# Kernel optimization log

Hardware: AMD Instinct MI355X
Metric: run time of the kernel (lower is better)

Reference implementation:

```python
import jax, jax.numpy as jnp
import numpy as np
import math

B, M, H, K, SPAN = 8, 1024, 512, 8, 1024
D = H // K
MK = M + SPAN


def _skew(X, pad_value):
    # shift every row one step to the right: [N, M, L] -> [N, M, M+L]
    N, m, L = X.shape
    X = jnp.pad(X, ((0, 0), (0, 0), (0, m + 1)), constant_values=pad_value)
    X = X.reshape(N, -1)[:, :-m]
    return X.reshape(N, m, m + L)


def _unskew(X):
    # reverse of _skew: [N, M, M+L] -> [N, M, L]
    N, m, Lk = X.shape
    L = Lk - m
    X = jnp.pad(X.reshape(N, -1), ((0, 0), (0, m)))
    return X.reshape(N, m, Lk + 1)[:, :, :L]


def setup_inputs() -> dict:
    key0 = jax.random.key(0)
    ks = jax.random.split(key0, 8)
    w_scale = 1.0 / math.sqrt(H)
    return {
        "query": jax.random.normal(ks[0], (B, M, H), jnp.float32),
        "key": jax.random.normal(ks[1], (B, MK, H), jnp.float32),
        "value": jax.random.normal(ks[2], (B, MK, H), jnp.float32),
        "pos_encoding": jax.random.normal(ks[3], (D, SPAN), jnp.float32) * w_scale,
        "Wq": jax.random.normal(ks[4], (H, H), jnp.float32) * w_scale,
        "Wk": jax.random.normal(ks[5], (H, H), jnp.float32) * w_scale,
        "Wv": jax.random.normal(ks[6], (H, H), jnp.float32) * w_scale,
        "Wo": jax.random.normal(ks[7], (H, H), jnp.float32) * w_scale,
    }


def _heads(x, W):
    # project then split heads: [B, T, H] -> [B*K, T, D]
    x = x @ W
    Bx, T, _ = x.shape
    x = x.reshape(Bx, T, K, D).transpose(0, 2, 1, 3)
    return x.reshape(Bx * K, T, D)


def reference(query, key, value, pos_encoding, Wq, Wk, Wv, Wo):
    q = _heads(query, Wq)      # [B*K, M, D]
    k = _heads(key, Wk)        # [B*K, MK, D]
    v = _heads(value, Wv)      # [B*K, MK, D]

    attn_ctx = jnp.einsum("nmd,nld->nml", q, k)   # [B*K, M, MK]
    attn_ctx = _unskew(attn_ctx)                    # [B*K, M, SPAN]
    attn_pos = jnp.einsum("nmd,ds->nms", q, pos_encoding)  # [B*K, M, SPAN]
    attn = jax.nn.softmax((attn_ctx + attn_pos) / math.sqrt(D), axis=-1)

    attn_sk = _skew(attn, 0.0)                      # [B*K, M, MK]
    out = jnp.einsum("nml,nld->nmd", attn_sk, v)   # [B*K, M, D]
    out = out.reshape(B, K, M, D).transpose(0, 2, 1, 3).reshape(B, M, H)
    return out @ Wo
```

## Files before the change

kernel.cpp:

```cpp
#include <hip/hip_runtime.h>
#include <stdint.h>

#define Bq 8
#define Mq 1024
#define Hq 512
#define NHq 8
#define Dq 64
#define SPANq 1024
#define MKq 2048
#define PR2 168

typedef __bf16 bf16x8 __attribute__((ext_vector_type(8)));
typedef _Float16 f16x8 __attribute__((ext_vector_type(8)));
typedef float f32x4 __attribute__((ext_vector_type(4)));
typedef unsigned short ushort8 __attribute__((ext_vector_type(8)));
typedef unsigned int uint2v __attribute__((ext_vector_type(2)));

static __device__ __forceinline__ unsigned short f2bf(float f) {
  union { float f; unsigned u; } x; x.f = f;
  unsigned r = x.u + 0x7FFFu + ((x.u >> 16) & 1u);
  return (unsigned short)(r >> 16);
}

static __device__ __forceinline__ unsigned pk_f16(float a, float b) {
  return __builtin_bit_cast(unsigned, __builtin_amdgcn_cvt_pkrtz(a, b));
}

static __device__ __forceinline__ f32x4 mfma_bf16(bf16x8 a, bf16x8 b, f32x4 c) {
  return __builtin_amdgcn_mfma_f32_16x16x32_bf16(a, b, c, 0, 0, 0);
}
static __device__ __forceinline__ f32x4 mfma_f16(f16x8 a, f16x8 b, f32x4 c) {
  return __builtin_amdgcn_mfma_f32_16x16x32_f16(a, b, c, 0, 0, 0);
}

static __device__ __forceinline__ void async_ld16(const void* g, void* l) {
  __builtin_amdgcn_global_load_lds(
      (const __attribute__((address_space(1))) void*)g,
      (__attribute__((address_space(3))) void*)l, 16, 0, 0);
}

__global__ __launch_bounds__(256) void prep_all(
    const float* __restrict__ query, const float* __restrict__ key,
    const float* __restrict__ value,
    const float* __restrict__ Wq, const float* __restrict__ Wk,
    const float* __restrict__ Wv, const float* __restrict__ Wo,
    const float* __restrict__ pos,
    unsigned short* __restrict__ qX, unsigned short* __restrict__ kX,
    unsigned short* __restrict__ vX,
    unsigned short* __restrict__ WTq, unsigned short* __restrict__ WTk,
    unsigned short* __restrict__ WTv, unsigned short* __restrict__ WTo,
    unsigned short* __restrict__ posT) {
  __shared__ float tile[64][65];
  const int bid = blockIdx.x;
  const int tid = threadIdx.x;
  if (bid >= 272) {
    const int rem = bid - 272;
    const float* src; unsigned short* dst; int off;
    if (rem < 2048)      { src = query; dst = qX; off = rem; }
    else if (rem < 6144) { src = key;   dst = kX; off = rem - 2048; }
    else                 { src = value; dst = vX; off = rem - 6144; }
    const int idx = off * 2048 + tid * 8;
    const f32x4 f0 = *(const f32x4*)(src + idx);
    const f32x4 f1 = *(const f32x4*)(src + idx + 4);
    ushort8 h;
    h[0] = f2bf(f0[0]); h[1] = f2bf(f0[1]); h[2] = f2bf(f0[2]); h[3] = f2bf(f0[3]);
    h[4] = f2bf(f1[0]); h[5] = f2bf(f1[1]); h[6] = f2bf(f1[2]); h[7] = f2bf(f1[3]);
    *(ushort8*)(dst + idx) = h;
    return;
  }
  const float* src; unsigned short* dst;
  int src_stride, dst_stride, i0, o0;
  if (bid < 256) {
    const int w = bid >> 6, t = bid & 63;
    src = (w == 0) ? Wq : (w == 1) ? Wk : (w == 2) ? Wv : Wo;
    dst = (w == 0) ? WTq : (w == 1) ? WTk : (w == 2) ? WTv : WTo;
    src_stride = Hq; dst_stride = Hq;
    i0 = (t >> 3) * 64; o0 = (t & 7) * 64;
  } else {
    const int t = bid - 256;
    src = pos; dst = posT;
    src_stride = SPANq; dst_stride = Dq;
    i0 = 0; o0 = t * 64;
  }
  for (int e = tid; e < 4096; e += 256) {
    const int r = e >> 6, c = e & 63;
    tile[r][c] = src[(size_t)(i0 + r) * src_stride + o0 + c];
  }
  __syncthreads();
  for (int e = tid; e < 4096; e += 256) {
    const int r = e >> 6, c = e & 63;
    dst[(size_t)(o0 + r) * dst_stride + i0 + c] = f2bf(tile[c][r]);
  }
}

static __device__ __forceinline__ void gemm_body(
    const unsigned short* __restrict__ Xb, const unsigned short* __restrict__ WT,
    unsigned short* __restrict__ outb, _Float16* __restrict__ outv,
    float* __restrict__ outf, int mode, int tshift, int bx, int by,
    unsigned short* sh) {
  unsigned short* As = sh;
  unsigned short* Bs = sh + 8192;
  const int tid = threadIdx.x;
  const int wave = tid >> 6, lane = tid & 63;
  const int q = lane >> 4, l16 = lane & 15;
  const int wy = wave >> 1, wx = wave & 1;
  const size_t m0 = (size_t)bx * 128;
  const int n0 = by * 128;
  const int dsub = lane >> 3;
  const int dswz = (lane & 7) ^ dsub;

  f32x4 acc[4][4] = {};

  for (int k0 = 0; k0 < Hq; k0 += 64) {
    __syncthreads();
#pragma unroll
    for (int i = 0; i < 4; i++) {
      const int s = wave * 4 + i;
      const int r = s * 8 + dsub;
      async_ld16(Xb + (m0 + r) * Hq + k0 + dswz * 8, As + s * 512);
      async_ld16(WT + (size_t)(n0 + r) * Hq + k0 + dswz * 8, Bs + s * 512);
    }
    __syncthreads();
#pragma unroll
    for (int h = 0; h < 2; h++) {
      bf16x8 af[4], bg[4];
#pragma unroll
      for (int mt = 0; mt < 4; mt++) {
        const int R = wy * 64 + mt * 16 + l16;
        af[mt] = *(const bf16x8*)(As + R * 64 + (((h * 4 + q) ^ (l16 & 7)) * 8));
      }
#pragma unroll
      for (int nt = 0; nt < 4; nt++) {
        const int R = wx * 64 + nt * 16 + l16;
        bg[nt] = *(const bf16x8*)(Bs + R * 64 + (((h * 4 + q) ^ (l16 & 7)) * 8));
      }
#pragma unroll
      for (int mt = 0; mt < 4; mt++)
#pragma unroll
        for (int nt = 0; nt < 4; nt++)
          acc[mt][nt] = mfma_bf16(af[mt], bg[nt], acc[mt][nt]);
    }
  }

  if (mode == 2) {
    __syncthreads();
    _Float16* tr = (_Float16*)sh + wave * 4608;
#pragma unroll
    for (int nt = 0; nt < 4; nt++)
#pragma unroll
      for (int mt = 0; mt < 4; mt++)
#pragma unroll
        for (int r = 0; r < 4; r++)
          tr[(nt * 16 + l16) * 72 + mt * 16 + q * 4 + r] = (_Float16)acc[mt][nt][r];
    const int head = by * 2 + wx;
    const int mrow0 = (int)m0 + wy * 64;
    const int Tlen = 1 << tshift;
    const int b = mrow0 >> tshift, t0 = mrow0 & (Tlen - 1);
#pragma unroll
    for (int it = 0; it < 8; it++) {
      const int dl = it * 8 + (lane >> 3), tl = (lane & 7) * 8;
      const f16x8 v = *(const f16x8*)(tr + dl * 72 + tl);
      *(f16x8*)(outv + ((size_t)((b * 8 + head) * 64 + dl)) * Tlen + t0 + tl) = v;
    }
    return;
  }

  const int Tlen = 1 << tshift;
#pragma unroll
  for (int mt = 0; mt < 4; mt++) {
#pragma unroll
    for (int nt = 0; nt < 4; nt++) {
      const int c = n0 + wx * 64 + nt * 16 + l16;
#pragma unroll
      for (int r = 0; r < 4; r++) {
        const int m = (int)m0 + wy * 64 + mt * 16 + q * 4 + r;
        const float val = acc[mt][nt][r];
        if (mode == 3) {
          outf[(size_t)m * Hq + c] = val;
        } else {
          const int b = m >> tshift, t = m & (Tlen - 1);
          const int head = c >> 6, d = c & 63;
          outb[(((size_t)(b * 8 + head) << tshift) + t) * 64 + d] = f2bf(val);
        }
      }
    }
  }
}

__global__ __launch_bounds__(256, 4) void gemm_qkv(
    const unsigned short* __restrict__ qX, const unsigned short* __restrict__ kX,
    const unsigned short* __restrict__ vX,
    const unsigned short* __restrict__ WTq, const unsigned short* __restrict__ WTk,
    const unsigned short* __restrict__ WTv,
    unsigned short* __restrict__ qb, unsigned short* __restrict__ kbuf,
    _Float16* __restrict__ vTb) {
  __shared__ unsigned short sh[18432];
  const int bid = blockIdx.x;
  if (bid < 256) {
    gemm_body(qX, WTq, qb, nullptr, nullptr, 0, 10, bid & 63, bid >> 6, sh);
  } else if (bid < 768) {
    const int b2 = bid - 256;
    gemm_body(kX, WTk, kbuf, nullptr, nullptr, 0, 11, b2 & 127, b2 >> 7, sh);
  } else {
    const int b2 = bid - 768;
    gemm_body(vX, WTv, nullptr, vTb, nullptr, 2, 11, b2 & 127, b2 >> 7, sh);
  }
}

__global__ __launch_bounds__(256, 4) void gemm_out(
    const unsigned short* __restrict__ ctx, const unsigned short* __restrict__ WTo,
    float* __restrict__ out) {
  __shared__ unsigned short sh[18432];
  const int bid = blockIdx.x;
  gemm_body(ctx, WTo, nullptr, nullptr, out, 3, 10, bid & 63, bid >> 6, sh);
}

__global__ __launch_bounds__(256, 2) void attn4(
    const unsigned short* __restrict__ qb, const unsigned short* __restrict__ kglob,
    const _Float16* __restrict__ vT, const unsigned short* __restrict__ posT,
    unsigned short* __restrict__ ctx) {
  __shared__ unsigned short Kt[12288];
  __shared__ unsigned short PosR[4 * 16 * PR2];
  __shared__ unsigned short Prow[4 * 16 * PR2];

  const int tid = threadIdx.x;
  const int wave = tid >> 6, lane = tid & 63;
  const int q = lane >> 4, l16 = lane & 15;
  const int bid = blockIdx.x;
  const int n = (bid & 7) * 8 + (bid >> 7);
  const int mtile = (bid >> 3) & 15;
  const int m0 = mtile * 64;
  const int m0w = m0 + wave * 16;
  const int dsub = lane >> 3;
  const int dswz = (lane & 7) ^ dsub;

  unsigned short* prow = Prow + (wave * 16 + l16) * PR2;
  unsigned short* posr = PosR + (wave * 16 + l16) * PR2;

  const unsigned short* qbase = qb + ((size_t)n * Mq + m0w + l16) * Dq;
  const bf16x8 qf0 = *(const bf16x8*)(qbase + q * 8);
  const bf16x8 qf1 = *(const bf16x8*)(qbase + 32 + q * 8);

  const unsigned short* kbn = kglob + (size_t)n * MKq * Dq;
  const _Float16* vbn = vT + (size_t)n * Dq * MKq;

  f32x4 O[4] = {};
  float zrow = 0.f, mrow = -1e30f;

#pragma unroll
  for (int i = 0; i < 6; i++) {
    const int s = wave + 4 * i;
    const int r = s * 8 + dsub;
    async_ld16(kbn + (size_t)(m0 + r) * Dq + dswz * 8, Kt + s * 512);
  }
  {
    bf16x8 pf[8][2];
#pragma unroll
    for (int t = 0; t < 8; t++) {
      const unsigned short* pp = posT + (size_t)(t * 16 + l16) * Dq + q * 8;
      pf[t][0] = *(const bf16x8*)pp;
      pf[t][1] = *(const bf16x8*)(pp + 32);
    }
#pragma unroll
    for (int t = 0; t < 8; t++) {
      f32x4 b = {};
      b = mfma_bf16(pf[t][0], qf0, b);
      b = mfma_bf16(pf[t][1], qf1, b);
      const int cw = 16 + t * 16 + 4 * q + l16;
      posr[cw + 0] = f2bf(b[0]);
      posr[cw + 1] = f2bf(b[1]);
      posr[cw + 2] = f2bf(b[2]);
      posr[cw + 3] = f2bf(b[3]);
    }
  }
  __syncthreads();

  for (int c = 0; c < 8; c++) {
    const int j00 = m0w + c * 128;

    f32x4 S[9];
#pragma unroll
    for (int t = 0; t < 9; t++) {
      const int rl = wave * 16 + t * 16 + l16;
      const int ch = (q ^ (l16 & 7)) * 8;
      const bf16x8 k0 = *(const bf16x8*)(Kt + rl * 64 + ch);
      const bf16x8 k1 = *(const bf16x8*)(Kt + rl * 64 + (ch ^ 32));
      f32x4 a = {};
      a = mfma_bf16(k0, qf0, a);
      a = mfma_bf16(k1, qf1, a);
      const uint2v pv = *(const uint2v*)(posr + 16 + t * 16 + 4 * q);
      a[0] += __uint_as_float(pv.x << 16);
      a[1] += __uint_as_float(pv.x & 0xffff0000u);
      a[2] += __uint_as_float(pv.y << 16);
      a[3] += __uint_as_float(pv.y & 0xffff0000u);
      S[t] = a;
    }
#pragma unroll
    for (int r = 0; r < 4; r++) {
      if (4 * q + r < l16) S[0][r] = -1e30f;
      if (4 * q + r >= l16) S[8][r] = -1e30f;
    }

    if (c < 7) {
      __syncthreads();
      const int jb1 = m0 + (c + 1) * 128;
#pragma unroll
      for (int i = 0; i < 6; i++) {
        const int s = wave + 4 * i;
        const int r = s * 8 + dsub;
        async_ld16(kbn + (size_t)(jb1 + r) * Dq + dswz * 8, Kt + s * 512);
      }
      const int sb1 = (c + 1) * 128;
      bf16x8 pf[8][2];
#pragma unroll
      for (int t = 0; t < 8; t++) {
        const unsigned short* pp = posT + (size_t)(sb1 + t * 16 + l16) * Dq + q * 8;
        pf[t][0] = *(const bf16x8*)pp;
        pf[t][1] = *(const bf16x8*)(pp + 32);
      }
#pragma unroll
      for (int t = 0; t < 8; t++) {
        f32x4 b = {};
        b = mfma_bf16(pf[t][0], qf0, b);
        b = mfma_bf16(pf[t][1], qf1, b);
        const int cw = 16 + t * 16 + 4 * q + l16;
        posr[cw + 0] = f2bf(b[0]);
        posr[cw + 1] = f2bf(b[1]);
        posr[cw + 2] = f2bf(b[2]);
        posr[cw + 3] = f2bf(b[3]);
      }
    }

    float mx = -1e30f;
#pragma unroll
    for (int t = 0; t < 9; t++)
      mx = fmaxf(mx, fmaxf(fmaxf(S[t][0], S[t][1]), fmaxf(S[t][2], S[t][3])));
    mx = fmaxf(mx, __shfl_xor(mx, 16, 64));
    mx = fmaxf(mx, __shfl_xor(mx, 32, 64));
    const float m_new = fmaxf(mrow, mx);
    const float alpha = __expf((mrow - m_new) * 0.125f);
    float zs = 0.f;
#pragma unroll
    for (int t = 0; t < 9; t++) {
#pragma unroll
      for (int r = 0; r < 4; r++) {
        const float e = __expf((S[t][r] - m_new) * 0.125f);
        S[t][r] = e; zs += e;
      }
    }
    zs += __shfl_xor(zs, 16, 64);
    zs += __shfl_xor(zs, 32, 64);
    zrow = zrow * alpha + zs;
    mrow = m_new;
#pragma unroll
    for (int dt = 0; dt < 4; dt++) O[dt] *= alpha;

#pragma unroll
    for (int t = 0; t < 9; t++) {
      *(unsigned*)(prow + t * 16 + 4 * q) = pk_f16(S[t][0], S[t][1]);
      *(unsigned*)(prow + t * 16 + 4 * q + 2) = pk_f16(S[t][2], S[t][3]);
    }
    *(unsigned*)(prow + 144 + 4 * q) = 0u;
    *(unsigned*)(prow + 144 + 4 * q + 2) = 0u;

    f16x8 Bf[5];
#pragma unroll
    for (int kt = 0; kt < 5; kt++)
      Bf[kt] = *(const f16x8*)(prow + kt * 32 + q * 8);
    f16x8 Vv[5][4];
#pragma unroll
    for (int kt = 0; kt < 5; kt++) {
      int j = j00 + kt * 32 + q * 8;
      if (j > MKq - 8) j = MKq - 8;
#pragma unroll
      for (int dt = 0; dt < 4; dt++)
        Vv[kt][dt] = *(const f16x8*)(vbn + (size_t)(dt * 16 + l16) * MKq + j);
    }
#pragma unroll
    for (int kt = 0; kt < 5; kt++)
#pragma unroll
      for (int dt = 0; dt < 4; dt++)
        O[dt] = mfma_f16(Vv[kt][dt], Bf[kt], O[dt]);

    if (c < 7) __syncthreads();
  }

  const float zi = 1.f / zrow;
  unsigned short* cp = ctx + ((size_t)(n >> 3) * Mq + m0w + l16) * Hq + (n & 7) * Dq;
#pragma unroll
  for (int dt = 0; dt < 4; dt++)
#pragma unroll
    for (int r = 0; r < 4; r++)
      cp[dt * 16 + q * 4 + r] = f2bf(O[dt][r] * zi);
}

extern "C" void kernel_launch(void* const* d_in, const int* in_sizes, int n_in,
                              void* d_out, int out_size, void* d_ws, size_t ws_size,
                              hipStream_t stream) {
  const float* query = (const float*)d_in[0];
  const float* key   = (const float*)d_in[1];
  const float* value = (const float*)d_in[2];
  const float* pos   = (const float*)d_in[3];
  const float* Wq    = (const float*)d_in[4];
  const float* Wk    = (const float*)d_in[5];
  const float* Wv    = (const float*)d_in[6];
  const float* Wo    = (const float*)d_in[7];
  float* out = (float*)d_out;

  char* w = (char*)d_ws;
  unsigned short* qX   = (unsigned short*)w; w += (size_t)Bq * Mq * Hq * 2;
  unsigned short* kX   = (unsigned short*)w; w += (size_t)Bq * MKq * Hq * 2;
  unsigned short* vX   = (unsigned short*)w; w += (size_t)Bq * MKq * Hq * 2;
  unsigned short* qb   = (unsigned short*)w; w += (size_t)64 * Mq * Dq * 2;
  unsigned short* kbuf = (unsigned short*)w; w += (size_t)64 * MKq * Dq * 2;
  _Float16*       vTb  = (_Float16*)w;       w += (size_t)64 * Dq * MKq * 2;
  unsigned short* posT = (unsigned short*)w; w += (size_t)SPANq * Dq * 2;
  unsigned short* WTq  = (unsigned short*)w; w += (size_t)Hq * Hq * 2;
  unsigned short* WTk  = (unsigned short*)w; w += (size_t)Hq * Hq * 2;
  unsigned short* WTv  = (unsigned short*)w; w += (size_t)Hq * Hq * 2;
  unsigned short* WTo  = (unsigned short*)w; w += (size_t)Hq * Hq * 2;
  unsigned short* ctx  = (unsigned short*)w; w += (size_t)Bq * Mq * Hq * 2;

  prep_all<<<10512, 256, 0, stream>>>(query, key, value, Wq, Wk, Wv, Wo, pos,
                                      qX, kX, vX, WTq, WTk, WTv, WTo, posT);
  gemm_qkv<<<1280, 256, 0, stream>>>(qX, kX, vX, WTq, WTk, WTv, qb, kbuf, vTb);
  attn4<<<1024, 256, 0, stream>>>(qb, kbuf, vTb, posT, ctx);
  gemm_out<<<256, 256, 0, stream>>>(ctx, WTo, out);
}
```

Measured before the change: 321.2 us.

## Drop shared K staging in attention, load K directly, raise occupancy

The attention kernel no longer stages K tiles into shared memory with async loads and block barriers. Each wave now reads its K rows straight from global memory into registers, and one shared row buffer serves both the position scores (now stored as fp16) and the probabilities. Loads are split into smaller groups to lower register pressure, and the launch bound rises to four blocks per CU. The GEMM inner loop is also reordered to keep fewer B fragments live. The aim is to remove barriers and LDS use in exchange for redundant global K reads across waves and lower precision for the position term.

Result: slower. 359.9 us (+12.1%).

```diff
diff --git a/kernel.cpp b/kernel.cpp
--- a/kernel.cpp
+++ b/kernel.cpp
@@ -24,6 +24,15 @@
 
 static __device__ __forceinline__ unsigned pk_f16(float a, float b) {
   return __builtin_bit_cast(unsigned, __builtin_amdgcn_cvt_pkrtz(a, b));
+}
+static __device__ __forceinline__ unsigned short f16b(float x) {
+  return __builtin_bit_cast(unsigned short, (_Float16)x);
+}
+static __device__ __forceinline__ float f16_lo(unsigned u) {
+  return (float)__builtin_bit_cast(_Float16, (unsigned short)(u & 0xffffu));
+}
+static __device__ __forceinline__ float f16_hi(unsigned u) {
+  return (float)__builtin_bit_cast(_Float16, (unsigned short)(u >> 16));
 }
 
 static __device__ __forceinline__ f32x4 mfma_bf16(bf16x8 a, bf16x8 b, f32x4 c) {
@@ -123,7 +132,7 @@
     __syncthreads();
 #pragma unroll
     for (int h = 0; h < 2; h++) {
-      bf16x8 af[4], bg[4];
+      bf16x8 af[4];
 #pragma unroll
       for (int mt = 0; mt < 4; mt++) {
         const int R = wy * 64 + mt * 16 + l16;
@@ -132,13 +141,11 @@
 #pragma unroll
       for (int nt = 0; nt < 4; nt++) {
         const int R = wx * 64 + nt * 16 + l16;
-        bg[nt] = *(const bf16x8*)(Bs + R * 64 + (((h * 4 + q) ^ (l16 & 7)) * 8));
-      }
-#pragma unroll
-      for (int mt = 0; mt < 4; mt++)
-#pragma unroll
-        for (int nt = 0; nt < 4; nt++)
-          acc[mt][nt] = mfma_bf16(af[mt], bg[nt], acc[mt][nt]);
+        const bf16x8 bg = *(const bf16x8*)(Bs + R * 64 + (((h * 4 + q) ^ (l16 & 7)) * 8));
+#pragma unroll
+        for (int mt = 0; mt < 4; mt++)
+          acc[mt][nt] = mfma_bf16(af[mt], bg, acc[mt][nt]);
+      }
     }
   }
 
@@ -215,13 +222,11 @@
   gemm_body(ctx, WTo, nullptr, nullptr, out, 3, 10, bid & 63, bid >> 6, sh);
 }
 
-__global__ __launch_bounds__(256, 2) void attn4(
+__global__ __launch_bounds__(256, 4) void attn5(
     const unsigned short* __restrict__ qb, const unsigned short* __restrict__ kglob,
     const _Float16* __restrict__ vT, const unsigned short* __restrict__ posT,
     unsigned short* __restrict__ ctx) {
-  __shared__ unsigned short Kt[12288];
-  __shared__ unsigned short PosR[4 * 16 * PR2];
-  __shared__ unsigned short Prow[4 * 16 * PR2];
+  __shared__ unsigned short Rows[4 * 16 * PR2];
 
   const int tid = threadIdx.x;
   const int wave = tid >> 6, lane = tid & 63;
@@ -229,13 +234,9 @@
   const int bid = blockIdx.x;
   const int n = (bid & 7) * 8 + (bid >> 7);
   const int mtile = (bid >> 3) & 15;
-  const int m0 = mtile * 64;
-  const int m0w = m0 + wave * 16;
-  const int dsub = lane >> 3;
-  const int dswz = (lane & 7) ^ dsub;
-
-  unsigned short* prow = Prow + (wave * 16 + l16) * PR2;
-  unsigned short* posr = PosR + (wave * 16 + l16) * PR2;
+  const int m0w = mtile * 64 + wave * 16;
+
+  unsigned short* row = Rows + (wave * 16 + l16) * PR2;
 
   const unsigned short* qbase = qb + ((size_t)n * Mq + m0w + l16) * Dq;
   const bf16x8 qf0 = *(const bf16x8*)(qbase + q * 8);
@@ -247,74 +248,15 @@
   f32x4 O[4] = {};
   float zrow = 0.f, mrow = -1e30f;
 
-#pragma unroll
-  for (int i = 0; i < 6; i++) {
-    const int s = wave + 4 * i;
-    const int r = s * 8 + dsub;
-    async_ld16(kbn + (size_t)(m0 + r) * Dq + dswz * 8, Kt + s * 512);
-  }
-  {
-    bf16x8 pf[8][2];
-#pragma unroll
-    for (int t = 0; t < 8; t++) {
-      const unsigned short* pp = posT + (size_t)(t * 16 + l16) * Dq + q * 8;
-      pf[t][0] = *(const bf16x8*)pp;
-      pf[t][1] = *(const bf16x8*)(pp + 32);
-    }
-#pragma unroll
-    for (int t = 0; t < 8; t++) {
-      f32x4 b = {};
-      b = mfma_bf16(pf[t][0], qf0, b);
-      b = mfma_bf16(pf[t][1], qf1, b);
-      const int cw = 16 + t * 16 + 4 * q + l16;
-      posr[cw + 0] = f2bf(b[0]);
-      posr[cw + 1] = f2bf(b[1]);
-      posr[cw + 2] = f2bf(b[2]);
-      posr[cw + 3] = f2bf(b[3]);
-    }
-  }
-  __syncthreads();
-
   for (int c = 0; c < 8; c++) {
-    const int j00 = m0w + c * 128;
-
-    f32x4 S[9];
-#pragma unroll
-    for (int t = 0; t < 9; t++) {
-      const int rl = wave * 16 + t * 16 + l16;
-      const int ch = (q ^ (l16 & 7)) * 8;
-      const bf16x8 k0 = *(const bf16x8*)(Kt + rl * 64 + ch);
-      const bf16x8 k1 = *(const bf16x8*)(Kt + rl * 64 + (ch ^ 32));
-      f32x4 a = {};
-      a = mfma_bf16(k0, qf0, a);
-      a = mfma_bf16(k1, qf1, a);
-      const uint2v pv = *(const uint2v*)(posr + 16 + t * 16 + 4 * q);
-      a[0] += __uint_as_float(pv.x << 16);
-      a[1] += __uint_as_float(pv.x & 0xffff0000u);
-      a[2] += __uint_as_float(pv.y << 16);
-      a[3] += __uint_as_float(pv.y & 0xffff0000u);
-      S[t] = a;
-    }
-#pragma unroll
-    for (int r = 0; r < 4; r++) {
-      if (4 * q + r < l16) S[0][r] = -1e30f;
-      if (4 * q + r >= l16) S[8][r] = -1e30f;
-    }
-
-    if (c < 7) {
-      __syncthreads();
-      const int jb1 = m0 + (c + 1) * 128;
-#pragma unroll
-      for (int i = 0; i < 6; i++) {
-        const int s = wave + 4 * i;
-        const int r = s * 8 + dsub;
-        async_ld16(kbn + (size_t)(jb1 + r) * Dq + dswz * 8, Kt + s * 512);
-      }
-      const int sb1 = (c + 1) * 128;
+    const int sbase = c * 128;
+    const int j00 = m0w + sbase;
+
+    {
       bf16x8 pf[8][2];
 #pragma unroll
       for (int t = 0; t < 8; t++) {
-        const unsigned short* pp = posT + (size_t)(sb1 + t * 16 + l16) * Dq + q * 8;
+        const unsigned short* pp = posT + (size_t)(sbase + t * 16 + l16) * Dq + q * 8;
         pf[t][0] = *(const bf16x8*)pp;
         pf[t][1] = *(const bf16x8*)(pp + 32);
       }
@@ -324,11 +266,59 @@
         b = mfma_bf16(pf[t][0], qf0, b);
         b = mfma_bf16(pf[t][1], qf1, b);
         const int cw = 16 + t * 16 + 4 * q + l16;
-        posr[cw + 0] = f2bf(b[0]);
-        posr[cw + 1] = f2bf(b[1]);
-        posr[cw + 2] = f2bf(b[2]);
-        posr[cw + 3] = f2bf(b[3]);
-      }
+        row[cw + 0] = f16b(b[0]);
+        row[cw + 1] = f16b(b[1]);
+        row[cw + 2] = f16b(b[2]);
+        row[cw + 3] = f16b(b[3]);
+      }
+    }
+
+    f32x4 S[9];
+    {
+      bf16x8 kf[5][2];
+#pragma unroll
+      for (int t = 0; t < 5; t++) {
+        const unsigned short* kp = kbn + (size_t)(j00 + t * 16 + l16) * Dq + q * 8;
+        kf[t][0] = *(const bf16x8*)kp;
+        kf[t][1] = *(const bf16x8*)(kp + 32);
+      }
+#pragma unroll
+      for (int t = 0; t < 5; t++) {
+        f32x4 a = {};
+        a = mfma_bf16(kf[t][0], qf0, a);
+        a = mfma_bf16(kf[t][1], qf1, a);
+        S[t] = a;
+      }
+    }
+    {
+      bf16x8 kg[4][2];
+#pragma unroll
+      for (int t = 0; t < 4; t++) {
+        const unsigned short* kp = kbn + (size_t)(j00 + (t + 5) * 16 + l16) * Dq + q * 8;
+        kg[t][0] = *(const bf16x8*)kp;
+        kg[t][1] = *(const bf16x8*)(kp + 32);
+      }
+#pragma unroll
+      for (int t = 0; t < 4; t++) {
+        f32x4 a = {};
+        a = mfma_bf16(kg[t][0], qf0, a);
+        a = mfma_bf16(kg[t][1], qf1, a);
+        S[t + 5] = a;
+      }
+    }
+
+#pragma unroll
+    for (int t = 0; t < 9; t++) {
+      const uint2v pv = *(const uint2v*)(row + 16 + t * 16 + 4 * q);
+      S[t][0] += f16_lo(pv.x);
+      S[t][1] += f16_hi(pv.x);
+      S[t][2] += f16_lo(pv.y);
+      S[t][3] += f16_hi(pv.y);
+    }
+#pragma unroll
+    for (int r = 0; r < 4; r++) {
+      if (4 * q + r < l16) S[0][r] = -1e30f;
+      if (4 * q + r >= l16) S[8][r] = -1e30f;
     }
 
     float mx = -1e30f;
@@ -357,32 +347,48 @@
 
 #pragma unroll
     for (int t = 0; t < 9; t++) {
-      *(unsigned*)(prow + t * 16 + 4 * q) = pk_f16(S[t][0], S[t][1]);
-      *(unsigned*)(prow + t * 16 + 4 * q + 2) = pk_f16(S[t][2], S[t][3]);
-    }
-    *(unsigned*)(prow + 144 + 4 * q) = 0u;
-    *(unsigned*)(prow + 144 + 4 * q + 2) = 0u;
+      *(unsigned*)(row + t * 16 + 4 * q) = pk_f16(S[t][0], S[t][1]);
+      *(unsigned*)(row + t * 16 + 4 * q + 2) = pk_f16(S[t][2], S[t][3]);
+    }
+    *(unsigned*)(row + 144 + 4 * q) = 0u;
+    *(unsigned*)(row + 144 + 4 * q + 2) = 0u;
 
     f16x8 Bf[5];
 #pragma unroll
     for (int kt = 0; kt < 5; kt++)
-      Bf[kt] = *(const f16x8*)(prow + kt * 32 + q * 8);
-    f16x8 Vv[5][4];
-#pragma unroll
-    for (int kt = 0; kt < 5; kt++) {
-      int j = j00 + kt * 32 + q * 8;
-      if (j > MKq - 8) j = MKq - 8;
-#pragma unroll
-      for (int dt = 0; dt < 4; dt++)
-        Vv[kt][dt] = *(const f16x8*)(vbn + (size_t)(dt * 16 + l16) * MKq + j);
-    }
-#pragma unroll
-    for (int kt = 0; kt < 5; kt++)
-#pragma unroll
-      for (int dt = 0; dt < 4; dt++)
-        O[dt] = mfma_f16(Vv[kt][dt], Bf[kt], O[dt]);
-
-    if (c < 7) __syncthreads();
+      Bf[kt] = *(const f16x8*)(row + kt * 32 + q * 8);
+    {
+      f16x8 Va[3][4];
+#pragma unroll
+      for (int kt = 0; kt < 3; kt++) {
+        int j = j00 + kt * 32 + q * 8;
+        if (j > MKq - 8) j = MKq - 8;
+#pragma unroll
+        for (int dt = 0; dt < 4; dt++)
+          Va[kt][dt] = *(const f16x8*)(vbn + (size_t)(dt * 16 + l16) * MKq + j);
+      }
+#pragma unroll
+      for (int kt = 0; kt < 3; kt++)
+#pragma unroll
+        for (int dt = 0; dt < 4; dt++)
+          O[dt] = mfma_f16(Va[kt][dt], Bf[kt], O[dt]);
+    }
+    {
+      f16x8 Vb[2][4];
+#pragma unroll
+      for (int kt = 0; kt < 2; kt++) {
+        int j = j00 + (kt + 3) * 32 + q * 8;
+        if (j > MKq - 8) j = MKq - 8;
+#pragma unroll
+        for (int dt = 0; dt < 4; dt++)
+          Vb[kt][dt] = *(const f16x8*)(vbn + (size_t)(dt * 16 + l16) * MKq + j);
+      }
+#pragma unroll
+      for (int kt = 0; kt < 2; kt++)
+#pragma unroll
+        for (int dt = 0; dt < 4; dt++)
+          O[dt] = mfma_f16(Vb[kt][dt], Bf[kt + 3], O[dt]);
+    }
   }
 
   const float zi = 1.f / zrow;
@@ -424,6 +430,6 @@
   prep_all<<<10512, 256, 0, stream>>>(query, key, value, Wq, Wk, Wv, Wo, pos,
                                       qX, kX, vX, WTq, WTk, WTv, WTo, posT);
   gemm_qkv<<<1280, 256, 0, stream>>>(qX, kX, vX, WTq, WTk, WTv, qb, kbuf, vTb);
-  attn4<<<1024, 256, 0, stream>>>(qb, kbuf, vTb, posT, ctx);
+  attn5<<<1024, 256, 0, stream>>>(qb, kbuf, vTb, posT, ctx);
   gemm_out<<<256, 256, 0, stream>>>(ctx, WTo, out);
 }
```
